# Optimization experiments

Hardware: AMD Instinct MI355X
Metric: run time of the kernel (lower is better)

Reference implementation:

```python
import jax, jax.numpy as jnp
import numpy as np

IN_F, OUT_F, NB = 4096, 4096, 8
BS = IN_F // NB  # 512


def setup_inputs() -> dict:
    key = jax.random.key(0)
    k1, k2, k3, k4 = jax.random.split(key, 4)
    weight = jax.random.normal(k1, (OUT_F, IN_F), dtype=jnp.float32) * 0.02
    bias = jax.random.normal(k2, (OUT_F,), dtype=jnp.float32) * 0.02
    x = jax.random.normal(k3, (4, 2048, IN_F), dtype=jnp.float32)
    R_blocks = jax.random.normal(k4, (NB, BS, BS), dtype=jnp.float32) * 0.1
    return {"weight": weight, "bias": bias, "x": x, "R_blocks": R_blocks, "layer_idx": 0}


def cayley_transform(A):
    # A: [nb, bs, bs]; Q = (I - A_skew) @ inv(I + A_skew + 1e-6 I)
    bs = A.shape[-1]
    I = jnp.eye(bs, dtype=A.dtype)
    A_skew = 0.5 * (A - jnp.swapaxes(A, -2, -1))
    return jnp.matmul(I - A_skew, jnp.linalg.inv(I + A_skew + 1e-6 * I))


def reference(weight, bias, x, R_blocks, layer_idx):
    R_ortho = cayley_transform(R_blocks)  # [nb, bs, bs]
    # weight @ block_diag(R) == per-block contraction on the in_features axis
    w = weight.reshape(OUT_F, NB, BS)
    tw = jnp.einsum('onb,nbc->onc', w, R_ortho).reshape(OUT_F, IN_F)
    # F.linear: x @ tw.T + bias
    out = jnp.einsum('bsi,oi->bso', x, tw) + bias
    return out
```

## Files before the change

### kernel.cpp

```cpp
#include <hip/hip_runtime.h>
#include <hip/hip_bf16.h>


typedef unsigned short u16;
typedef __attribute__((ext_vector_type(8))) __bf16 bf16x8;
typedef __attribute__((ext_vector_type(4))) float f32x4;
typedef __attribute__((ext_vector_type(8))) unsigned short u16x8;
typedef __attribute__((ext_vector_type(4))) unsigned short u16x4;

#define C0   1.000001f
#define C1Q  2.000001f
#define AS1 __attribute__((address_space(1)))
#define AS3 __attribute__((address_space(3)))

__device__ __forceinline__ u16 f2bf(float x) {
  union { float f; unsigned u; } v; v.f = x;
  return (u16)((v.u + 0x7fffu + ((v.u >> 16) & 1u)) >> 16);
}
__device__ __forceinline__ float bf2f(u16 h) {
  union { float f; unsigned u; } v; v.u = ((unsigned)h) << 16; return v.f;
}

__global__ __launch_bounds__(256) void k_build_M(const float* __restrict__ R,
                                                 u16* __restrict__ Mh,
                                                 u16* __restrict__ Ml) {
  __shared__ float t1[32][33];
  const int n = blockIdx.z;
  const int tr = blockIdx.y * 32, tc = blockIdx.x * 32;
  const int ly = threadIdx.x >> 5, lx = threadIdx.x & 31;
  const float* Rb = R + (size_t)n * 262144;
  float a[4];
#pragma unroll
  for (int i = 0; i < 4; ++i) {
    a[i] = Rb[(size_t)(tr + ly + i * 8) * 512 + tc + lx];
    t1[ly + i * 8][lx] = Rb[(size_t)(tc + ly + i * 8) * 512 + tr + lx];
  }
  __syncthreads();
#pragma unroll
  for (int i = 0; i < 4; ++i) {
    const int r = tr + ly + i * 8, c = tc + lx;
    float m = 0.5f * (a[i] - t1[lx][ly + i * 8]) + (r == c ? C0 : 0.0f);
    u16 h = f2bf(m);
    const size_t idx = (size_t)n * 262144 + (size_t)r * 512 + c;
    Mh[idx] = h;
    Ml[idx] = f2bf(m - bf2f(h));
  }
}

__global__ __launch_bounds__(1024) void k_frob_alpha(const u16* __restrict__ G4,
                                                     float* __restrict__ coef) {
  __shared__ float red[16];
  const int n = blockIdx.x, tid = threadIdx.x;
  const u16* src = G4 + (size_t)n * 262144;
  float s = 0.f;
  for (int i = tid; i < 32768; i += 1024) {
    u16x8 v = reinterpret_cast<const u16x8*>(src)[i];
#pragma unroll
    for (int e = 0; e < 8; ++e) { float f = bf2f(v[e]); s += f * f; }
  }
  for (int off = 32; off; off >>= 1) s += __shfl_down(s, off, 64);
  if ((tid & 63) == 0) red[tid >> 6] = s;
  __syncthreads();
  if (tid == 0) {
    float t = 0.f;
    for (int q = 0; q < 16; ++q) t += red[q];
    float lam = powf(t, 0.125f);
    float a = 2.0f / (C0 * C0 + lam);
    coef[n] = a;
    float e = (lam - C0 * C0) / (lam + C0 * C0);
    float sq = e * e;
    float c1 = 2.0f / (2.0f - sq);
    coef[8 + n]  = 2.0f * c1;
    coef[16 + n] = -c1 * a;
    coef[24 + n] = 2.0f * c1 * a;
    coef[32 + n] = -c1 * a * a;
    e = sq / (2.0f - sq);
    sq = e * e;
    float c2 = 2.0f / (2.0f - sq);
    coef[40 + n] = 2.0f * c2;
    coef[48 + n] = -c2;
    e = sq / (2.0f - sq);
    sq = e * e;
    float c3 = 2.0f / (2.0f - sq);
    coef[56 + n] = 2.0f * c3;
    coef[64 + n] = -c3;
  }
}

__global__ __launch_bounds__(256) void k_init(const u16* __restrict__ Mh,
                                              const u16* __restrict__ Ml,
                                              const u16* __restrict__ G,
                                              const u16* __restrict__ G2,
                                              const float* __restrict__ coef,
                                              u16* __restrict__ X0,
                                              u16* __restrict__ T2) {
  int idx = blockIdx.x * 256 + threadIdx.x;
  int n = idx >> 18, r = (idx >> 9) & 511, c = idx & 511;
  float m = bf2f(Mh[idx]) + bf2f(Ml[idx]);
  X0[idx] = f2bf(coef[n] * ((r == c ? 2.0f * C0 : 0.0f) - m));
  T2[idx] = f2bf(coef[24 + n] * bf2f(G[idx]) + coef[32 + n] * bf2f(G2[idx]));
}

#define BMM_FRAGS(rs)                                                          \
  bf16x8 a[2], b[2], al2[2], bl2[2];                                           \
  _Pragma("unroll")                                                            \
  for (int i = 0; i < 2; ++i) {                                                \
    const int fr = wr * 32 + i * 16 + c15;                                     \
    const int ia = (rs) * 2048 + fr * 32 + ((lk ^ (fr & 3)) * 8);              \
    a[i] = *reinterpret_cast<const bf16x8*>(&sA[ia]);                          \
    if constexpr (PROD3) al2[i] = *reinterpret_cast<const bf16x8*>(&sAl[ia]);  \
  }                                                                            \
  _Pragma("unroll")                                                            \
  for (int j = 0; j < 2; ++j) {                                                \
    const int fc = wc * 32 + j * 16 + c15;                                     \
    const int ib = (rs) * 2048 + fc * 32 + ((lk ^ (fc & 3)) * 8);              \
    b[j] = *reinterpret_cast<const bf16x8*>(&sB[ib]);                          \
    if constexpr (PROD3) bl2[j] = *reinterpret_cast<const bf16x8*>(&sBl[ib]);  \
  }                                                                            \
  _Pragma("unroll")                                                            \
  for (int i = 0; i < 2; ++i)                                                  \
    _Pragma("unroll")                                                          \
    for (int j = 0; j < 2; ++j) {                                              \
      acc[i][j] = __builtin_amdgcn_mfma_f32_16x16x32_bf16(a[i], b[j], acc[i][j], 0, 0, 0); \
      if constexpr (PROD3) {                                                   \
        acc[i][j] = __builtin_amdgcn_mfma_f32_16x16x32_bf16(a[i],   bl2[j], acc[i][j], 0, 0, 0); \
        acc[i][j] = __builtin_amdgcn_mfma_f32_16x16x32_bf16(al2[i], b[j],   acc[i][j], 0, 0, 0); \
      }                                                                        \
    }

#define BMM_WAIT(SEL)                                                          \
  if ((SEL) == 0) {                                                            \
    if constexpr (PROD3) asm volatile("s_waitcnt vmcnt(8)" ::: "memory");      \
    else                 asm volatile("s_waitcnt vmcnt(4)" ::: "memory");      \
  } else if ((SEL) == 1) {                                                     \
    if constexpr (PROD3) asm volatile("s_waitcnt vmcnt(4)" ::: "memory");      \
    else                 asm volatile("s_waitcnt vmcnt(2)" ::: "memory");      \
  } else {                                                                     \
    asm volatile("s_waitcnt vmcnt(0)" ::: "memory");                           \
  }

template <int PROD3, int DMODE, int OMODE, int DUAL>
__global__ __launch_bounds__(256)
void k_bmm(const u16* __restrict__ Ah, const u16* __restrict__ Al,
           const u16* __restrict__ Bh, const u16* __restrict__ Bl,
           const u16* __restrict__ Dh, const u16* __restrict__ Dl,
           u16* __restrict__ Cnh, u16* __restrict__ Cnl,
           u16* __restrict__ Cth, u16* __restrict__ Ctl,
           float cd, float cs,
           const float* __restrict__ cdp, const float* __restrict__ csp,
           const float* __restrict__ cvsrc, u16* __restrict__ cvdst, int zmm,
           const u16* __restrict__ A2, const u16* __restrict__ B2,
           const u16* __restrict__ D2, u16* __restrict__ C2) {
  __shared__ __align__(16) u16 sA[4 * 2048], sB[4 * 2048];
  __shared__ __align__(16) u16 sAl[PROD3 ? 4 * 2048 : 8];
  __shared__ __align__(16) u16 sBl[PROD3 ? 4 * 2048 : 8];

  if ((int)blockIdx.z >= zmm) {
    const int zi = ((int)blockIdx.z - zmm) * 64 + blockIdx.y * 8 + blockIdx.x;
    const int chunk = zi >> 7;
    const int base = (zi & 127) * 256 + (int)threadIdx.x;
    const float* src = cvsrc + (size_t)chunk * 4194304;
    u16* dst = cvdst + (size_t)chunk * 4194304;
#pragma unroll
    for (int e = 0; e < 16; ++e) {
      const size_t g = (size_t)(base + e * 32768) * 8;
      float4 f0 = *reinterpret_cast<const float4*>(src + g);
      float4 f1 = *reinterpret_cast<const float4*>(src + g + 4);
      u16x8 w;
      w[0] = f2bf(f0.x); w[1] = f2bf(f0.y); w[2] = f2bf(f0.z); w[3] = f2bf(f0.w);
      w[4] = f2bf(f1.x); w[5] = f2bf(f1.y); w[6] = f2bf(f1.z); w[7] = f2bf(f1.w);
      *reinterpret_cast<u16x8*>(dst + g) = w;
    }
    return;
  }

  const int zq = DUAL ? ((blockIdx.z >> 3) & 1) : 0;
  const u16* Ah_ = (DUAL && zq) ? A2 : Ah;
  const u16* Bh_ = (DUAL && zq) ? B2 : Bh;
  const u16* Dh_ = (DUAL && zq) ? D2 : Dh;
  u16* Cnh_ = (DUAL && zq) ? C2 : Cnh;
  const size_t zb = (size_t)(blockIdx.z & 7) * 262144;
  const int tid = threadIdx.x, lane = tid & 63, wave = tid >> 6;
  const int m0 = blockIdx.y * 64, n0 = blockIdx.x * 64;
  const int wr = wave >> 1, wc = wave & 1;
  const int c15 = lane & 15, lk = lane >> 4;
  const int srow = tid >> 2;
  const int sg = (tid & 3) ^ (srow & 3);
  f32x4 acc[2][2] = {};
  const u16* pa = Ah_ + zb + (size_t)(m0 + srow) * 512 + sg * 8;
  const u16* pb = Bh_ + zb + (size_t)(n0 + srow) * 512 + sg * 8;
  const u16* pal = PROD3 ? Al + zb + (size_t)(m0 + srow) * 512 + sg * 8 : pa;
  const u16* pbl = PROD3 ? Bl + zb + (size_t)(n0 + srow) * 512 + sg * 8 : pb;

  int jn = 0, js = 0;
  auto STG = [&]() {
    if (jn < 16) {
      const int off = jn << 5;
      __builtin_amdgcn_global_load_lds((const AS1 void*)(pa + off),
                                       (AS3 void*)(sA + js * 2048 + tid * 8), 16, 0, 0);
      __builtin_amdgcn_global_load_lds((const AS1 void*)(pb + off),
                                       (AS3 void*)(sB + js * 2048 + tid * 8), 16, 0, 0);
      if constexpr (PROD3) {
        __builtin_amdgcn_global_load_lds((const AS1 void*)(pal + off),
                                         (AS3 void*)(sAl + js * 2048 + tid * 8), 16, 0, 0);
        __builtin_amdgcn_global_load_lds((const AS1 void*)(pbl + off),
                                         (AS3 void*)(sBl + js * 2048 + tid * 8), 16, 0, 0);
      }
    }
    ++jn; js = (js + 1) & 3;
  };

  STG(); STG();
  int rs = 0;
  for (int t = 0; t < 14; ++t) {
    STG();
    BMM_WAIT(0)
    __builtin_amdgcn_s_barrier();
    BMM_FRAGS(rs)
    rs = (rs + 1) & 3;
  }
  STG();
  BMM_WAIT(1)
  __builtin_amdgcn_s_barrier();
  { BMM_FRAGS(rs) }
  rs = (rs + 1) & 3;
  STG();
  BMM_WAIT(2)
  __builtin_amdgcn_s_barrier();
  { BMM_FRAGS(rs) }

  const float cdL = cdp ? cdp[blockIdx.z & 7] : cd;
  const float csL = csp ? csp[blockIdx.z & 7] : cs;
#pragma unroll
  for (int i = 0; i < 2; ++i)
#pragma unroll
    for (int j = 0; j < 2; ++j) {
      const int rowb = m0 + wr * 32 + i * 16 + lk * 4;
      const int col  = n0 + wc * 32 + j * 16 + c15;
      u16 hv[4], lv[4];
#pragma unroll
      for (int r = 0; r < 4; ++r) {
        float val = csL * acc[i][j][r];
        if constexpr (DMODE >= 1) {
          float d = bf2f(Dh_[zb + (size_t)(rowb + r) * 512 + col]);
          if constexpr (DMODE == 2) d += bf2f(Dl[zb + (size_t)(rowb + r) * 512 + col]);
          val += cdL * d;
        }
        u16 h = f2bf(val);
        if constexpr (OMODE & 1) Cnh_[zb + (size_t)(rowb + r) * 512 + col] = h;
        u16 l = 0;
        if constexpr (OMODE & 10) l = f2bf(val - bf2f(h));
        if constexpr (OMODE & 2) Cnl[zb + (size_t)(rowb + r) * 512 + col] = l;
        hv[r] = h; lv[r] = l;
      }
      if constexpr (OMODE & 4) {
        u16x4 v; v[0] = hv[0]; v[1] = hv[1]; v[2] = hv[2]; v[3] = hv[3];
        *reinterpret_cast<u16x4*>(&Cth[zb + (size_t)col * 512 + rowb]) = v;
      }
      if constexpr (OMODE & 8) {
        u16x4 v; v[0] = lv[0]; v[1] = lv[1]; v[2] = lv[2]; v[3] = lv[3];
        *reinterpret_cast<u16x4*>(&Ctl[zb + (size_t)col * 512 + rowb]) = v;
      }
    }
}

__global__ __launch_bounds__(256)
void k_twmm(const u16* __restrict__ W, const u16* __restrict__ Qt,
            u16* __restrict__ tw) {
  __shared__ __align__(16) u16 sA[4 * 2048], sB[4 * 2048];
  const int z = blockIdx.z;
  const size_t zb = (size_t)z * 262144;
  const int tid = threadIdx.x, lane = tid & 63, wave = tid >> 6;
  const int m0 = blockIdx.y * 64, n0 = blockIdx.x * 64;
  const int wr = wave >> 1, wc = wave & 1;
  const int c15 = lane & 15, lk = lane >> 4;
  const int srow = tid >> 2;
  const int sg = (tid & 3) ^ (srow & 3);
  f32x4 acc[2][2] = {};
  const u16* pa = W + (size_t)(m0 + srow) * 4096 + z * 512 + sg * 8;
  const u16* pb = Qt + zb + (size_t)(n0 + srow) * 512 + sg * 8;

  int jn = 0, js = 0;
  auto STG = [&]() {
    if (jn < 16) {
      const int off = jn << 5;
      __builtin_amdgcn_global_load_lds((const AS1 void*)(pa + off),
                                       (AS3 void*)(sA + js * 2048 + tid * 8), 16, 0, 0);
      __builtin_amdgcn_global_load_lds((const AS1 void*)(pb + off),
                                       (AS3 void*)(sB + js * 2048 + tid * 8), 16, 0, 0);
    }
    ++jn; js = (js + 1) & 3;
  };

#define TW_FRAGS(rs)                                                           \
  {                                                                            \
    bf16x8 a[2], b[2];                                                         \
    _Pragma("unroll")                                                          \
    for (int i = 0; i < 2; ++i) {                                              \
      const int fr = wr * 32 + i * 16 + c15;                                   \
      a[i] = *reinterpret_cast<const bf16x8*>(                                 \
          &sA[(rs) * 2048 + fr * 32 + ((lk ^ (fr & 3)) * 8)]);                 \
    }                                                                          \
    _Pragma("unroll")                                                          \
    for (int j = 0; j < 2; ++j) {                                              \
      const int fc = wc * 32 + j * 16 + c15;                                   \
      b[j] = *reinterpret_cast<const bf16x8*>(                                 \
          &sB[(rs) * 2048 + fc * 32 + ((lk ^ (fc & 3)) * 8)]);                 \
    }                                                                          \
    _Pragma("unroll")                                                          \
    for (int i = 0; i < 2; ++i)                                                \
      _Pragma("unroll")                                                        \
      for (int j = 0; j < 2; ++j)                                              \
        acc[i][j] = __builtin_amdgcn_mfma_f32_16x16x32_bf16(a[i], b[j], acc[i][j], 0, 0, 0); \
  }

  STG(); STG();
  int rs = 0;
  for (int t = 0; t < 14; ++t) {
    STG();
    asm volatile("s_waitcnt vmcnt(4)" ::: "memory");
    __builtin_amdgcn_s_barrier();
    TW_FRAGS(rs)
    rs = (rs + 1) & 3;
  }
  STG();
  asm volatile("s_waitcnt vmcnt(2)" ::: "memory");
  __builtin_amdgcn_s_barrier();
  TW_FRAGS(rs)
  rs = (rs + 1) & 3;
  STG();
  asm volatile("s_waitcnt vmcnt(0)" ::: "memory");
  __builtin_amdgcn_s_barrier();
  TW_FRAGS(rs)

#pragma unroll
  for (int i = 0; i < 2; ++i)
#pragma unroll
    for (int j = 0; j < 2; ++j) {
      const int rowb = m0 + wr * 32 + i * 16 + lk * 4;
      const int col  = z * 512 + n0 + wc * 32 + j * 16 + c15;
#pragma unroll
      for (int r = 0; r < 4; ++r)
        tw[(size_t)(rowb + r) * 4096 + col] = f2bf(acc[i][j][r]);
    }
}

#define NSL 18

#define RD_A3(dst, MH)                                                         \
  _Pragma("unroll")                                                            \
  for (int m = 0; m < 4; ++m)                                                  \
    dst[m] = *reinterpret_cast<const bf16x8*>(                                 \
        &lds[aslot * 4096 + ((MH) * 64 + m * 16 + c15) * 32 + gsw * 8]);

#define RD_B3(dst)                                                             \
  _Pragma("unroll")                                                            \
  for (int n = 0; n < 4; ++n)                                                  \
    dst[n] = *reinterpret_cast<const bf16x8*>(                                 \
        &lds[bslot * 4096 + (bq64 + n * 16 + c15) * 32 + gsw * 8]);

#define MFMA16(afX, bfX, MH)                                                   \
  __builtin_amdgcn_s_setprio(1);                                               \
  _Pragma("unroll")                                                            \
  for (int m = 0; m < 4; ++m)                                                  \
    _Pragma("unroll")                                                          \
    for (int n = 0; n < 4; ++n)                                                \
      acc[(MH) * 4 + m][n] = __builtin_amdgcn_mfma_f32_16x16x32_bf16(          \
          afX[m], bfX[n], acc[(MH) * 4 + m][n], 0, 0, 0);                      \
  __builtin_amdgcn_s_setprio(0);

#define TILE32(WM)                                                             \
  {                                                                            \
    int aslot = s0 + wr;            if (aslot >= NSL) aslot -= NSL;            \
    int bslot = s0 + 2 + (wc >> 1); if (bslot >= NSL) bslot -= NSL;            \
    STAGE(); STAGE();                                                          \
    RD_B3(bfr)                                                                 \
    RD_A3(afA, 0)                                                              \
    MFMA16(afA, bfr, 0)                                                        \
    STAGE(); STAGE();                                                          \
    RD_A3(afB, 1)                                                              \
    MFMA16(afB, bfr, 1)                                                        \
    if ((WM) == 1) asm volatile("s_waitcnt vmcnt(8)" ::: "memory");            \
    if ((WM) == 2) asm volatile("s_waitcnt vmcnt(4)" ::: "memory");            \
    if ((WM) == 3) asm volatile("s_waitcnt vmcnt(0)" ::: "memory");            \
    if ((WM) != 0) {                                                           \
      __builtin_amdgcn_s_barrier();                                            \
      __builtin_amdgcn_sched_barrier(0);                                       \
    }                                                                          \
    s0 += 4; if (s0 >= NSL) s0 -= NSL;                                         \
  }

__global__ __launch_bounds__(512, 2)
void k_gemm256(const u16* __restrict__ A, const u16* __restrict__ B,
               const float* __restrict__ bias,
               float* __restrict__ C, int N, int K) {
  __shared__ __align__(16) u16 lds[NSL * 4096];
  const int tid = threadIdx.x, lane = tid & 63, wave = tid >> 6;
  int bid = blockIdx.y * gridDim.x + blockIdx.x;
  const int cpx = (gridDim.x * gridDim.y) >> 3;
  bid = (bid & 7) * cpx + (bid >> 3);
  const int nbx = N >> 8;
  const int bx = bid % nbx, by = bid / nbx;
  const int m0 = by << 8, n0 = bx << 8;
  const int wr = wave >> 2, wc = wave & 3;
  const int srow = tid >> 2;
  const int sgc  = (tid & 3) ^ ((srow >> 1) & 3);
  const int c15 = lane & 15, lq = lane >> 4;
  const int gsw = lq ^ ((c15 >> 1) & 3);
  const int bq64 = (wc & 1) * 64;
  const int NT = K >> 5;

  f32x4 acc[8][4] = {};
  bf16x8 afA[4], afB[4], bfr[4];

  int jn = 0, js = 0;
  auto STAGE = [&]() {
    if (jn < 4 * NT) {
      const int t = jn >> 2, q = jn & 3;
      const u16* srcb = (q < 2)
          ? A + (size_t)(m0 + q * 128 + srow) * (size_t)K
          : B + (size_t)(n0 + (q - 2) * 128 + srow) * (size_t)K;
      const u16* src = srcb + (t << 5) + sgc * 8;
      u16* dst = (u16*)lds + js * 4096 + tid * 8;
      __builtin_amdgcn_global_load_lds(
          (const AS1 void*)src, (AS3 void*)dst, 16, 0, 0);
    }
    ++jn; js = (js == NSL - 1) ? 0 : js + 1;
  };

#pragma unroll
  for (int i = 0; i < 12; ++i) STAGE();
  asm volatile("s_waitcnt vmcnt(8)" ::: "memory");
  __builtin_amdgcn_s_barrier();
  __builtin_amdgcn_sched_barrier(0);

  int s0 = 0;
  for (int tau = 0; tau < NT - 3; ++tau) {
    TILE32(1)
  }
  TILE32(2)
  TILE32(3)
  TILE32(0)

#pragma unroll
  for (int n = 0; n < 4; ++n) {
    const int col = n0 + wc * 64 + n * 16 + c15;
    const float bv = bias[col];
#pragma unroll
    for (int mi = 0; mi < 8; ++mi) {
      const int rowb = m0 + wr * 128 + mi * 16 + (lq << 2);
#pragma unroll
      for (int r = 0; r < 4; ++r)
        C[(size_t)(rowb + r) * N + col] = acc[mi][n][r] + bv;
    }
  }
}

extern "C" void kernel_launch(void* const* d_in, const int* in_sizes, int n_in,
                              void* d_out, int out_size, void* d_ws, size_t ws_size,
                              hipStream_t stream) {
  const float* W    = (const float*)d_in[0];
  const float* bias = (const float*)d_in[1];
  const float* x    = (const float*)d_in[2];
  const float* R    = (const float*)d_in[3];
  float* out = (float*)d_out;

  char* ws = (char*)d_ws;
  u16* x_bf = (u16*)(ws);
  u16* tw   = (u16*)(ws + 67108864);
  u16* W_bf = (u16*)(ws + 100663296);

  char* arena = (char*)d_out;
  auto slot = [&](int i) -> u16* { return (u16*)(arena + (size_t)i * 4194304); };
  u16 *Mh = slot(0), *Ml = slot(1);
  u16 *G = slot(2), *G2 = slot(3), *G4 = slot(4);
  u16 *X0 = slot(5), *T2 = slot(6), *X1 = slot(7), *X2 = slot(8), *T3 = slot(9);
  u16 *X3h = slot(10), *X3l = slot(11), *X3th = slot(12), *X3tl = slot(13);
  u16 *Tpth = slot(14), *Tptl = slot(15);
  u16 *X4h = slot(16), *X4l = slot(17), *X4th = slot(18), *X4tl = slot(19);
  u16 *Qt = slot(20);
  float* coef = (float*)(arena + (size_t)21 * 4194304);

  const u16* NUL = nullptr;
  const float* NULF = nullptr;
  u16* NULW = nullptr;
  const dim3 gC1(8, 8, 10);
  const dim3 gC2(8, 8, 12);

  k_build_M<<<dim3(16, 16, 8), 256, 0, stream>>>(R, Mh, Ml);
  k_bmm<0, 0, 1, 0><<<gC1, 256, 0, stream>>>(Mh, NUL, Mh, NUL, NUL, NUL,
      G, NULW, NULW, NULW, 0.f, 1.f, NULF, NULF, W, W_bf, 8, NUL, NUL, NUL, NULW);
  k_bmm<0, 0, 1, 0><<<gC1, 256, 0, stream>>>(G, NUL, G, NUL, NUL, NUL,
      G2, NULW, NULW, NULW, 0.f, 1.f, NULF, NULF,
      W + 4194304, W_bf + 4194304, 8, NUL, NUL, NUL, NULW);
  k_bmm<0, 0, 1, 0><<<gC1, 256, 0, stream>>>(G2, NUL, G2, NUL, NUL, NUL,
      G4, NULW, NULW, NULW, 0.f, 1.f, NULF, NULF,
      W + 2 * 4194304, W_bf + 2 * 4194304, 8, NUL, NUL, NUL, NULW);
  k_frob_alpha<<<8, 1024, 0, stream>>>(G4, coef);
  k_init<<<8192, 256, 0, stream>>>(Mh, Ml, G, G2, coef, X0, T2);
  k_bmm<0, 1, 1, 0><<<gC1, 256, 0, stream>>>(X0, NUL, G, NUL, X0, NUL,
      X1, NULW, NULW, NULW, 0.f, 0.f, coef + 8, coef + 16,
      W + 3 * 4194304, W_bf + 3 * 4194304, 8, NUL, NUL, NUL, NULW);
  k_bmm<0, 1, 1, 1><<<dim3(8, 8, 20), 256, 0, stream>>>(X1, NUL, T2, NUL, X1, NUL,
      X2, NULW, NULW, NULW, 0.f, 0.f, coef + 40, coef + 48,
      x, x_bf, 16, T2, T2, T2, T3);
  k_bmm<0, 1, 15, 0><<<gC2, 256, 0, stream>>>(X2, NUL, T3, NUL, X2, NUL,
      X3h, X3l, X3th, X3tl, 0.f, 0.f, coef + 56, coef + 64,
      x + (size_t)2 * 4194304, x_bf + (size_t)2 * 4194304, 8, NUL, NUL, NUL, NULW);
  k_bmm<1, 0, 12, 0><<<gC2, 256, 0, stream>>>(Mh, Ml, X3th, X3tl, NUL, NUL,
      NULW, NULW, Tpth, Tptl, 0.f, 1.f, NULF, NULF,
      x + (size_t)4 * 4194304, x_bf + (size_t)4 * 4194304, 8, NUL, NUL, NUL, NULW);
  k_bmm<1, 2, 15, 0><<<gC1, 256, 0, stream>>>(X3h, X3l, Tpth, Tptl, X3h, X3l,
      X4h, X4l, X4th, X4tl, 2.f, -1.f, NULF, NULF,
      x + (size_t)6 * 4194304, x_bf + (size_t)6 * 4194304, 8, NUL, NUL, NUL, NULW);
  k_bmm<1, 2, 4, 0><<<gC1, 256, 0, stream>>>(Mh, Ml, X4th, X4tl, X4h, X4l,
      NULW, NULW, Qt, NULW, C1Q, -1.f, NULF, NULF,
      x + (size_t)7 * 4194304, x_bf + (size_t)7 * 4194304, 8, NUL, NUL, NUL, NULW);
  k_twmm<<<dim3(8, 64, 8), 256, 0, stream>>>(W_bf, Qt, tw);
  k_gemm256<<<dim3(16, 32), 512, 0, stream>>>(x_bf, tw, bias, out, 4096, 4096);
}
```

Baseline: 520.8 us.

## Drop G4 squaring by estimating spectral scale from G2 and rebalance conversion work

The norm estimate for the Newton-Schulz style inverse now uses the Frobenius norm of G2 raised to 1/4 instead of G4 to 1/8. This removes one batched 512x512 matmul (the G2·G2 squaring) from the chain of serialized launches. The fused fp32-to-bf16 conversion work for W and x, which rides on the bmm launches as extra grid z-slices, is redistributed across the remaining kernels. The last two bmm launches carry no conversion slices. The looser norm bound may give a less tight initial scaling, which could hurt convergence accuracy of the iteration.

New measurement: 502.9 us. -3.4%, faster.

```diff
diff --git a/kernel.cpp b/kernel.cpp
--- a/kernel.cpp
+++ b/kernel.cpp
@@ -47,11 +47,11 @@
   }
 }
 
-__global__ __launch_bounds__(1024) void k_frob_alpha(const u16* __restrict__ G4,
+__global__ __launch_bounds__(1024) void k_frob_alpha(const u16* __restrict__ G2,
                                                      float* __restrict__ coef) {
   __shared__ float red[16];
   const int n = blockIdx.x, tid = threadIdx.x;
-  const u16* src = G4 + (size_t)n * 262144;
+  const u16* src = G2 + (size_t)n * 262144;
   float s = 0.f;
   for (int i = tid; i < 32768; i += 1024) {
     u16x8 v = reinterpret_cast<const u16x8*>(src)[i];
@@ -64,7 +64,7 @@
   if (tid == 0) {
     float t = 0.f;
     for (int q = 0; q < 16; ++q) t += red[q];
-    float lam = powf(t, 0.125f);
+    float lam = powf(t, 0.25f);
     float a = 2.0f / (C0 * C0 + lam);
     coef[n] = a;
     float e = (lam - C0 * C0) / (lam + C0 * C0);
@@ -473,7 +473,7 @@
   char* arena = (char*)d_out;
   auto slot = [&](int i) -> u16* { return (u16*)(arena + (size_t)i * 4194304); };
   u16 *Mh = slot(0), *Ml = slot(1);
-  u16 *G = slot(2), *G2 = slot(3), *G4 = slot(4);
+  u16 *G = slot(2), *G2 = slot(3);
   u16 *X0 = slot(5), *T2 = slot(6), *X1 = slot(7), *X2 = slot(8), *T3 = slot(9);
   u16 *X3h = slot(10), *X3l = slot(11), *X3th = slot(12), *X3tl = slot(13);
   u16 *Tpth = slot(14), *Tptl = slot(15);
@@ -484,38 +484,35 @@
   const u16* NUL = nullptr;
   const float* NULF = nullptr;
   u16* NULW = nullptr;
-  const dim3 gC1(8, 8, 10);
+  const dim3 gC0(8, 8, 8);
   const dim3 gC2(8, 8, 12);
 
   k_build_M<<<dim3(16, 16, 8), 256, 0, stream>>>(R, Mh, Ml);
-  k_bmm<0, 0, 1, 0><<<gC1, 256, 0, stream>>>(Mh, NUL, Mh, NUL, NUL, NUL,
+  k_bmm<0, 0, 1, 0><<<gC2, 256, 0, stream>>>(Mh, NUL, Mh, NUL, NUL, NUL,
       G, NULW, NULW, NULW, 0.f, 1.f, NULF, NULF, W, W_bf, 8, NUL, NUL, NUL, NULW);
-  k_bmm<0, 0, 1, 0><<<gC1, 256, 0, stream>>>(G, NUL, G, NUL, NUL, NUL,
+  k_bmm<0, 0, 1, 0><<<gC2, 256, 0, stream>>>(G, NUL, G, NUL, NUL, NUL,
       G2, NULW, NULW, NULW, 0.f, 1.f, NULF, NULF,
-      W + 4194304, W_bf + 4194304, 8, NUL, NUL, NUL, NULW);
-  k_bmm<0, 0, 1, 0><<<gC1, 256, 0, stream>>>(G2, NUL, G2, NUL, NUL, NUL,
-      G4, NULW, NULW, NULW, 0.f, 1.f, NULF, NULF,
-      W + 2 * 4194304, W_bf + 2 * 4194304, 8, NUL, NUL, NUL, NULW);
-  k_frob_alpha<<<8, 1024, 0, stream>>>(G4, coef);
+      W + (size_t)2 * 4194304, W_bf + (size_t)2 * 4194304, 8, NUL, NUL, NUL, NULW);
+  k_frob_alpha<<<8, 1024, 0, stream>>>(G2, coef);
   k_init<<<8192, 256, 0, stream>>>(Mh, Ml, G, G2, coef, X0, T2);
-  k_bmm<0, 1, 1, 0><<<gC1, 256, 0, stream>>>(X0, NUL, G, NUL, X0, NUL,
+  k_bmm<0, 1, 1, 0><<<gC2, 256, 0, stream>>>(X0, NUL, G, NUL, X0, NUL,
       X1, NULW, NULW, NULW, 0.f, 0.f, coef + 8, coef + 16,
-      W + 3 * 4194304, W_bf + 3 * 4194304, 8, NUL, NUL, NUL, NULW);
+      x, x_bf, 8, NUL, NUL, NUL, NULW);
   k_bmm<0, 1, 1, 1><<<dim3(8, 8, 20), 256, 0, stream>>>(X1, NUL, T2, NUL, X1, NUL,
       X2, NULW, NULW, NULW, 0.f, 0.f, coef + 40, coef + 48,
-      x, x_bf, 16, T2, T2, T2, T3);
+      x + (size_t)2 * 4194304, x_bf + (size_t)2 * 4194304, 16, T2, T2, T2, T3);
   k_bmm<0, 1, 15, 0><<<gC2, 256, 0, stream>>>(X2, NUL, T3, NUL, X2, NUL,
       X3h, X3l, X3th, X3tl, 0.f, 0.f, coef + 56, coef + 64,
-      x + (size_t)2 * 4194304, x_bf + (size_t)2 * 4194304, 8, NUL, NUL, NUL, NULW);
+      x + (size_t)4 * 4194304, x_bf + (size_t)4 * 4194304, 8, NUL, NUL, NUL, NULW);
   k_bmm<1, 0, 12, 0><<<gC2, 256, 0, stream>>>(Mh, Ml, X3th, X3tl, NUL, NUL,
       NULW, NULW, Tpth, Tptl, 0.f, 1.f, NULF, NULF,
-      x + (size_t)4 * 4194304, x_bf + (size_t)4 * 4194304, 8, NUL, NUL, NUL, NULW);
-  k_bmm<1, 2, 15, 0><<<gC1, 256, 0, stream>>>(X3h, X3l, Tpth, Tptl, X3h, X3l,
+      x + (size_t)6 * 4194304, x_bf + (size_t)6 * 4194304, 8, NUL, NUL, NUL, NULW);
+  k_bmm<1, 2, 15, 0><<<gC0, 256, 0, stream>>>(X3h, X3l, Tpth, Tptl, X3h, X3l,
       X4h, X4l, X4th, X4tl, 2.f, -1.f, NULF, NULF,
-      x + (size_t)6 * 4194304, x_bf + (size_t)6 * 4194304, 8, NUL, NUL, NUL, NULW);
-  k_bmm<1, 2, 4, 0><<<gC1, 256, 0, stream>>>(Mh, Ml, X4th, X4tl, X4h, X4l,
+      x, x_bf, 8, NUL, NUL, NUL, NULW);
+  k_bmm<1, 2, 4, 0><<<gC0, 256, 0, stream>>>(Mh, Ml, X4th, X4tl, X4h, X4l,
       NULW, NULW, Qt, NULW, C1Q, -1.f, NULF, NULF,
-      x + (size_t)7 * 4194304, x_bf + (size_t)7 * 4194304, 8, NUL, NUL, NUL, NULW);
+      x, x_bf, 8, NUL, NUL, NUL, NULW);
   k_twmm<<<dim3(8, 64, 8), 256, 0, stream>>>(W_bf, Qt, tw);
   k_gemm256<<<dim3(16, 32), 512, 0, stream>>>(x_bf, tw, bias, out, 4096, 4096);
 }
```
